# Kernel tuning notes

Measured on AMD Instinct MI355X. Metric: run time of the kernel, lower is better.

Reference implementation:

```python
import jax, jax.numpy as jnp
import numpy as np

H = 1024      # hidden_size
V = 50257     # output_size (vocab)
L = 512       # max_length


def setup_inputs() -> dict:
    key = jax.random.key(0)
    ks = jax.random.split(key, 12)
    s = 0.02
    return {
        "x": jax.random.randint(ks[0], (1,), 0, V),
        "encoder_outputs": jax.random.normal(ks[1], (L, H), jnp.float32),
        "hidden": jax.random.normal(ks[2], (1, 1, H), jnp.float32),
        # parameters
        "emb": jax.random.normal(ks[3], (V, H), jnp.float32) * s,
        "attn_W": jax.random.normal(ks[4], (L, 2 * H), jnp.float32) * s,
        "attn_b": jnp.zeros((L,), jnp.float32),
        "comb_W": jax.random.normal(ks[5], (H, 2 * H), jnp.float32) * s,
        "comb_b": jnp.zeros((H,), jnp.float32),
        "W_ih": jax.random.normal(ks[6], (3 * H, H), jnp.float32) * s,
        "W_hh": jax.random.normal(ks[7], (3 * H, H), jnp.float32) * s,
        "b_ih": jnp.zeros((3 * H,), jnp.float32),
        "b_hh": jnp.zeros((3 * H,), jnp.float32),
        "out_W": jax.random.normal(ks[8], (V, H), jnp.float32) * s,
        "out_b": jnp.zeros((V,), jnp.float32),
    }


def reference(x, encoder_outputs, hidden, emb, attn_W, attn_b, comb_W, comb_b,
              W_ih, W_hh, b_ih, b_hh, out_W, out_b):
    # embedded: [1, H]  (dropout_p=0 -> identity)
    embedded = emb[x]
    h0 = hidden[0]  # [1, H]
    # Bahdanau-style attention over encoder positions
    attn_weights = jax.nn.softmax(
        jnp.concatenate([embedded, h0], axis=1) @ attn_W.T + attn_b, axis=1)  # [1, L]
    attn_applied = attn_weights @ encoder_outputs  # [1, H]
    # combine + relu
    out = jnp.concatenate([embedded, attn_applied], axis=1) @ comb_W.T + comb_b
    out = jax.nn.relu(out)  # [1, H] -- GRU input
    # GRU cell (PyTorch gate ordering: r, z, n)
    gx = out @ W_ih.T + b_ih   # [1, 3H]
    gh = h0 @ W_hh.T + b_hh    # [1, 3H]
    gx_r, gx_z, gx_n = jnp.split(gx, 3, axis=1)
    gh_r, gh_z, gh_n = jnp.split(gh, 3, axis=1)
    r = jax.nn.sigmoid(gx_r + gh_r)
    z = jax.nn.sigmoid(gx_z + gh_z)
    n = jnp.tanh(gx_n + r * gh_n)
    h_new = (1.0 - z) * n + z * h0  # [1, H]
    # output projection + log_softmax
    logp = jax.nn.log_softmax(h_new @ out_W.T + out_b, axis=1)  # [1, V]
    return logp, attn_weights
```

## Files before the change

kernel.cpp:

```cpp
#include <hip/hip_runtime.h>
#include <math.h>

#define H 1024
#define V 50257
#define L 512

__device__ inline float wave_reduce_sum(float v) {
    #pragma unroll
    for (int off = 32; off > 0; off >>= 1)
        v += __shfl_down(v, off, 64);
    return v;
}

__device__ inline float wave_reduce_max(float v) {
    #pragma unroll
    for (int off = 32; off > 0; off >>= 1)
        v = fmaxf(v, __shfl_down(v, off, 64));
    return v;
}

__global__ void scores_kernel(const int* __restrict__ x,
                              const float* __restrict__ emb,
                              const float* __restrict__ hidden,
                              const float* __restrict__ attn_W,
                              const float* __restrict__ attn_b,
                              float* __restrict__ scores) {
    const int l = blockIdx.x;
    const int t = threadIdx.x;
    const int xi = x[0];
    const float* wrow = attn_W + (size_t)l * (2 * H);
    float acc = 0.f;
    #pragma unroll
    for (int k = 0; k < 8; ++k) {
        int j = t + k * 256;
        float a = (j < H) ? emb[(size_t)xi * H + j] : hidden[j - H];
        acc += a * wrow[j];
    }
    __shared__ float sm[4];
    acc = wave_reduce_sum(acc);
    if ((t & 63) == 0) sm[t >> 6] = acc;
    __syncthreads();
    if (t == 0)
        scores[l] = sm[0] + sm[1] + sm[2] + sm[3] + attn_b[l];
}

__global__ void softmax512(const float* __restrict__ scores,
                           float* __restrict__ attnw,
                           float* __restrict__ out_attn) {
    const int t = threadIdx.x;
    __shared__ float sm[8];
    float v = scores[t];
    float m = wave_reduce_max(v);
    if ((t & 63) == 0) sm[t >> 6] = m;
    __syncthreads();
    float M = sm[0];
    #pragma unroll
    for (int i = 1; i < 8; ++i) M = fmaxf(M, sm[i]);
    float e = expf(v - M);
    __syncthreads();
    float s = wave_reduce_sum(e);
    if ((t & 63) == 0) sm[t >> 6] = s;
    __syncthreads();
    float S = 0.f;
    #pragma unroll
    for (int i = 0; i < 8; ++i) S += sm[i];
    float w = e / S;
    attnw[t] = w;
    out_attn[t] = w;
}

__global__ void attn_apply(const float* __restrict__ attnw,
                           const float* __restrict__ enc,
                           float* __restrict__ attnap) {
    const int h = blockIdx.x * blockDim.x + threadIdx.x;
    float acc = 0.f;
    for (int l = 0; l < L; ++l)
        acc += attnw[l] * enc[(size_t)l * H + h];
    attnap[h] = acc;
}

__global__ void combine_relu(const int* __restrict__ x,
                             const float* __restrict__ emb,
                             const float* __restrict__ attnap,
                             const float* __restrict__ comb_W,
                             const float* __restrict__ comb_b,
                             float* __restrict__ gru_in) {
    const int r = blockIdx.x;
    const int t = threadIdx.x;
    const int xi = x[0];
    const float* wrow = comb_W + (size_t)r * (2 * H);
    float acc = 0.f;
    #pragma unroll
    for (int k = 0; k < 8; ++k) {
        int j = t + k * 256;
        float a = (j < H) ? emb[(size_t)xi * H + j] : attnap[j - H];
        acc += a * wrow[j];
    }
    __shared__ float sm[4];
    acc = wave_reduce_sum(acc);
    if ((t & 63) == 0) sm[t >> 6] = acc;
    __syncthreads();
    if (t == 0)
        gru_in[r] = fmaxf(sm[0] + sm[1] + sm[2] + sm[3] + comb_b[r], 0.f);
}

__global__ void gates_kernel(const float* __restrict__ W_ih,
                             const float* __restrict__ W_hh,
                             const float* __restrict__ b_ih,
                             const float* __restrict__ b_hh,
                             const float* __restrict__ gru_in,
                             const float* __restrict__ hidden,
                             float* __restrict__ gx,
                             float* __restrict__ gh) {
    const int b = blockIdx.x;
    const int t = threadIdx.x;
    const float* w;
    const float* vec;
    float bias;
    float* outp;
    int r;
    if (b < 3 * H) {
        r = b; w = W_ih + (size_t)r * H; vec = gru_in; bias = b_ih[r]; outp = gx;
    } else {
        r = b - 3 * H; w = W_hh + (size_t)r * H; vec = hidden; bias = b_hh[r]; outp = gh;
    }
    float acc = 0.f;
    #pragma unroll
    for (int k = 0; k < 4; ++k) {
        int j = t + k * 256;
        acc += vec[j] * w[j];
    }
    __shared__ float sm[4];
    acc = wave_reduce_sum(acc);
    if ((t & 63) == 0) sm[t >> 6] = acc;
    __syncthreads();
    if (t == 0)
        outp[r] = sm[0] + sm[1] + sm[2] + sm[3] + bias;
}

__global__ void gru_cell(const float* __restrict__ gx,
                         const float* __restrict__ gh,
                         const float* __restrict__ hidden,
                         float* __restrict__ h_new) {
    const int i = blockIdx.x * blockDim.x + threadIdx.x;
    float r = 1.f / (1.f + expf(-(gx[i] + gh[i])));
    float z = 1.f / (1.f + expf(-(gx[H + i] + gh[H + i])));
    float n = tanhf(gx[2 * H + i] + r * gh[2 * H + i]);
    h_new[i] = (1.f - z) * n + z * hidden[i];
}

__global__ void logits_kernel(const float* __restrict__ out_W,
                              const float* __restrict__ out_b,
                              const float* __restrict__ h_new,
                              float* __restrict__ logits) {
    const int lid = threadIdx.x & 63;
    const int wid = threadIdx.x >> 6;
    const int v = blockIdx.x * 4 + wid;
    if (v >= V) return;
    const float4* wrow = (const float4*)(out_W + (size_t)v * H);
    const float4* hv = (const float4*)h_new;
    float acc = 0.f;
    #pragma unroll
    for (int it = 0; it < 4; ++it) {
        int idx = it * 64 + lid;
        float4 w = wrow[idx];
        float4 h = hv[idx];
        acc += w.x * h.x + w.y * h.y + w.z * h.z + w.w * h.w;
    }
    acc = wave_reduce_sum(acc);
    if (lid == 0)
        logits[v] = acc + out_b[v];
}

__global__ void logsumexp_kernel(const float* __restrict__ logits,
                                 float* __restrict__ red) {
    const int t = threadIdx.x;
    __shared__ float sm[16];
    float m = -INFINITY;
    for (int v = t; v < V; v += 1024) m = fmaxf(m, logits[v]);
    m = wave_reduce_max(m);
    if ((t & 63) == 0) sm[t >> 6] = m;
    __syncthreads();
    float M = sm[0];
    #pragma unroll
    for (int i = 1; i < 16; ++i) M = fmaxf(M, sm[i]);
    __syncthreads();
    float s = 0.f;
    for (int v = t; v < V; v += 1024) s += expf(logits[v] - M);
    s = wave_reduce_sum(s);
    if ((t & 63) == 0) sm[t >> 6] = s;
    __syncthreads();
    if (t == 0) {
        float S = 0.f;
        #pragma unroll
        for (int i = 0; i < 16; ++i) S += sm[i];
        red[0] = M + logf(S);
    }
}

__global__ void finalize_kernel(float* __restrict__ logits,
                                const float* __restrict__ red) {
    const int v = blockIdx.x * blockDim.x + threadIdx.x;
    if (v < V) logits[v] -= red[0];
}

extern "C" void kernel_launch(void* const* d_in, const int* in_sizes, int n_in,
                              void* d_out, int out_size, void* d_ws, size_t ws_size,
                              hipStream_t stream) {
    const int*   x       = (const int*)d_in[0];
    const float* enc     = (const float*)d_in[1];
    const float* hidden  = (const float*)d_in[2];
    const float* emb     = (const float*)d_in[3];
    const float* attn_W  = (const float*)d_in[4];
    const float* attn_b  = (const float*)d_in[5];
    const float* comb_W  = (const float*)d_in[6];
    const float* comb_b  = (const float*)d_in[7];
    const float* W_ih    = (const float*)d_in[8];
    const float* W_hh    = (const float*)d_in[9];
    const float* b_ih    = (const float*)d_in[10];
    const float* b_hh    = (const float*)d_in[11];
    const float* out_W   = (const float*)d_in[12];
    const float* out_b   = (const float*)d_in[13];
    float* out = (float*)d_out;
    float* ws  = (float*)d_ws;

    float* scores = ws;
    float* attnw  = ws + 512;
    float* attnap = ws + 1024;
    float* gru_in = ws + 2048;
    float* gx     = ws + 3072;
    float* gh     = ws + 6144;
    float* h_new  = ws + 9216;
    float* red    = ws + 10240;

    scores_kernel<<<L, 256, 0, stream>>>(x, emb, hidden, attn_W, attn_b, scores);
    softmax512<<<1, L, 0, stream>>>(scores, attnw, out + V);
    attn_apply<<<H / 256, 256, 0, stream>>>(attnw, enc, attnap);
    combine_relu<<<H, 256, 0, stream>>>(x, emb, attnap, comb_W, comb_b, gru_in);
    gates_kernel<<<6 * H, 256, 0, stream>>>(W_ih, W_hh, b_ih, b_hh, gru_in, hidden, gx, gh);
    gru_cell<<<H / 256, 256, 0, stream>>>(gx, gh, hidden, h_new);
    logits_kernel<<<(V + 3) / 4, 256, 0, stream>>>(out_W, out_b, h_new, out);
    logsumexp_kernel<<<1, 1024, 0, stream>>>(out, red);
    finalize_kernel<<<(V + 255) / 256, 256, 0, stream>>>(out, red);
}
```

Measured before the change: 450.6 us.

## Fuse log-softmax partials into logits, split attention-apply over L, vectorize GEMVs

The logits kernel now computes 16 rows per block and writes a per-block (max, sum-exp) partial. This drops the single-block logsumexp pass over all 50K logits. Each finalize block reduces the ~3K partials redundantly and then subtracts the log-normalizer. attn_apply is split across 8 L-chunks with atomicAdd into a buffer that the softmax kernel zeroes, and the small GEMVs switch to float4 loads. The trade-offs are redundant partial reduction in every finalize block and nondeterministic float atomics.

```diff
diff --git a/kernel.cpp b/kernel.cpp
--- a/kernel.cpp
+++ b/kernel.cpp
@@ -4,6 +4,7 @@
 #define H 1024
 #define V 50257
 #define L 512
+#define NPART ((V + 15) / 16)
 
 __device__ inline float wave_reduce_sum(float v) {
     #pragma unroll
@@ -17,6 +18,10 @@
     for (int off = 32; off > 0; off >>= 1)
         v = fmaxf(v, __shfl_down(v, off, 64));
     return v;
+}
+
+__device__ inline float dot4(float4 a, float4 b) {
+    return a.x * b.x + a.y * b.y + a.z * b.z + a.w * b.w;
 }
 
 __global__ void scores_kernel(const int* __restrict__ x,
@@ -28,14 +33,10 @@
     const int l = blockIdx.x;
     const int t = threadIdx.x;
     const int xi = x[0];
-    const float* wrow = attn_W + (size_t)l * (2 * H);
-    float acc = 0.f;
-    #pragma unroll
-    for (int k = 0; k < 8; ++k) {
-        int j = t + k * 256;
-        float a = (j < H) ? emb[(size_t)xi * H + j] : hidden[j - H];
-        acc += a * wrow[j];
-    }
+    const float4* wrow = (const float4*)(attn_W + (size_t)l * (2 * H));
+    const float4* ev = (const float4*)(emb + (size_t)xi * H);
+    const float4* hv = (const float4*)hidden;
+    float acc = dot4(ev[t], wrow[t]) + dot4(hv[t], wrow[t + 256]);
     __shared__ float sm[4];
     acc = wave_reduce_sum(acc);
     if ((t & 63) == 0) sm[t >> 6] = acc;
@@ -46,8 +47,11 @@
 
 __global__ void softmax512(const float* __restrict__ scores,
                            float* __restrict__ attnw,
-                           float* __restrict__ out_attn) {
-    const int t = threadIdx.x;
+                           float* __restrict__ out_attn,
+                           float* __restrict__ attnap) {
+    const int t = threadIdx.x;
+    attnap[t] = 0.f;
+    attnap[t + 512] = 0.f;
     __shared__ float sm[8];
     float v = scores[t];
     float m = wave_reduce_max(v);
@@ -72,11 +76,13 @@
 __global__ void attn_apply(const float* __restrict__ attnw,
                            const float* __restrict__ enc,
                            float* __restrict__ attnap) {
-    const int h = blockIdx.x * blockDim.x + threadIdx.x;
+    const int h = blockIdx.x * 256 + threadIdx.x;
+    const int l0 = blockIdx.y * 64;
     float acc = 0.f;
-    for (int l = 0; l < L; ++l)
-        acc += attnw[l] * enc[(size_t)l * H + h];
-    attnap[h] = acc;
+    #pragma unroll 8
+    for (int i = 0; i < 64; ++i)
+        acc += attnw[l0 + i] * enc[(size_t)(l0 + i) * H + h];
+    atomicAdd(&attnap[h], acc);
 }
 
 __global__ void combine_relu(const int* __restrict__ x,
@@ -88,14 +94,10 @@
     const int r = blockIdx.x;
     const int t = threadIdx.x;
     const int xi = x[0];
-    const float* wrow = comb_W + (size_t)r * (2 * H);
-    float acc = 0.f;
-    #pragma unroll
-    for (int k = 0; k < 8; ++k) {
-        int j = t + k * 256;
-        float a = (j < H) ? emb[(size_t)xi * H + j] : attnap[j - H];
-        acc += a * wrow[j];
-    }
+    const float4* wrow = (const float4*)(comb_W + (size_t)r * (2 * H));
+    const float4* ev = (const float4*)(emb + (size_t)xi * H);
+    const float4* av = (const float4*)attnap;
+    float acc = dot4(ev[t], wrow[t]) + dot4(av[t], wrow[t + 256]);
     __shared__ float sm[4];
     acc = wave_reduce_sum(acc);
     if ((t & 63) == 0) sm[t >> 6] = acc;
@@ -124,12 +126,7 @@
     } else {
         r = b - 3 * H; w = W_hh + (size_t)r * H; vec = hidden; bias = b_hh[r]; outp = gh;
     }
-    float acc = 0.f;
-    #pragma unroll
-    for (int k = 0; k < 4; ++k) {
-        int j = t + k * 256;
-        acc += vec[j] * w[j];
-    }
+    float acc = dot4(((const float4*)vec)[t], ((const float4*)w)[t]);
     __shared__ float sm[4];
     acc = wave_reduce_sum(acc);
     if ((t & 63) == 0) sm[t >> 6] = acc;
@@ -152,56 +149,64 @@
 __global__ void logits_kernel(const float* __restrict__ out_W,
                               const float* __restrict__ out_b,
                               const float* __restrict__ h_new,
-                              float* __restrict__ logits) {
+                              float* __restrict__ logits,
+                              float* __restrict__ partials) {
     const int lid = threadIdx.x & 63;
     const int wid = threadIdx.x >> 6;
-    const int v = blockIdx.x * 4 + wid;
-    if (v >= V) return;
-    const float4* wrow = (const float4*)(out_W + (size_t)v * H);
+    __shared__ float sl[16];
     const float4* hv = (const float4*)h_new;
-    float acc = 0.f;
-    #pragma unroll
-    for (int it = 0; it < 4; ++it) {
-        int idx = it * 64 + lid;
-        float4 w = wrow[idx];
-        float4 h = hv[idx];
-        acc += w.x * h.x + w.y * h.y + w.z * h.z + w.w * h.w;
+    float4 h0 = hv[lid], h1 = hv[64 + lid], h2 = hv[128 + lid], h3 = hv[192 + lid];
+    const int vbase = blockIdx.x * 16 + wid * 4;
+    #pragma unroll
+    for (int rr = 0; rr < 4; ++rr) {
+        const int v = vbase + rr;
+        float val = -INFINITY;
+        if (v < V) {
+            const float4* wr = (const float4*)(out_W + (size_t)v * H);
+            float acc = dot4(wr[lid], h0) + dot4(wr[64 + lid], h1)
+                      + dot4(wr[128 + lid], h2) + dot4(wr[192 + lid], h3);
+            acc = wave_reduce_sum(acc);
+            if (lid == 0) { val = acc + out_b[v]; logits[v] = val; }
+        }
+        if (lid == 0) sl[wid * 4 + rr] = val;
     }
-    acc = wave_reduce_sum(acc);
-    if (lid == 0)
-        logits[v] = acc + out_b[v];
-}
-
-__global__ void logsumexp_kernel(const float* __restrict__ logits,
-                                 float* __restrict__ red) {
-    const int t = threadIdx.x;
-    __shared__ float sm[16];
+    __syncthreads();
+    if (threadIdx.x == 0) {
+        float M = -INFINITY;
+        #pragma unroll
+        for (int i = 0; i < 16; ++i) M = fmaxf(M, sl[i]);
+        float S = 0.f;
+        #pragma unroll
+        for (int i = 0; i < 16; ++i) S += expf(sl[i] - M);
+        partials[2 * blockIdx.x] = M;
+        partials[2 * blockIdx.x + 1] = S;
+    }
+}
+
+__global__ void finalize_kernel(float* __restrict__ logits,
+                                const float* __restrict__ partials) {
+    const int t = threadIdx.x;
+    __shared__ float sm[8];
     float m = -INFINITY;
-    for (int v = t; v < V; v += 1024) m = fmaxf(m, logits[v]);
+    for (int i = t; i < NPART; i += 512) m = fmaxf(m, partials[2 * i]);
     m = wave_reduce_max(m);
     if ((t & 63) == 0) sm[t >> 6] = m;
     __syncthreads();
     float M = sm[0];
     #pragma unroll
-    for (int i = 1; i < 16; ++i) M = fmaxf(M, sm[i]);
+    for (int i = 1; i < 8; ++i) M = fmaxf(M, sm[i]);
     __syncthreads();
     float s = 0.f;
-    for (int v = t; v < V; v += 1024) s += expf(logits[v] - M);
+    for (int i = t; i < NPART; i += 512) s += partials[2 * i + 1] * expf(partials[2 * i] - M);
     s = wave_reduce_sum(s);
     if ((t & 63) == 0) sm[t >> 6] = s;
     __syncthreads();
-    if (t == 0) {
-        float S = 0.f;
-        #pragma unroll
-        for (int i = 0; i < 16; ++i) S += sm[i];
-        red[0] = M + logf(S);
-    }
-}
-
-__global__ void finalize_kernel(float* __restrict__ logits,
-                                const float* __restrict__ red) {
-    const int v = blockIdx.x * blockDim.x + threadIdx.x;
-    if (v < V) logits[v] -= red[0];
+    float S = 0.f;
+    #pragma unroll
+    for (int i = 0; i < 8; ++i) S += sm[i];
+    const float red = M + logf(S);
+    const int v = blockIdx.x * 512 + t;
+    if (v < V) logits[v] -= red;
 }
 
 extern "C" void kernel_launch(void* const* d_in, const int* in_sizes, int n_in,
@@ -224,22 +229,21 @@
     float* out = (float*)d_out;
     float* ws  = (float*)d_ws;
 
-    float* scores = ws;
-    float* attnw  = ws + 512;
-    float* attnap = ws + 1024;
-    float* gru_in = ws + 2048;
-    float* gx     = ws + 3072;
-    float* gh     = ws + 6144;
-    float* h_new  = ws + 9216;
-    float* red    = ws + 10240;
+    float* scores   = ws;
+    float* attnw    = ws + 512;
+    float* attnap   = ws + 1024;
+    float* gru_in   = ws + 2048;
+    float* gx       = ws + 3072;
+    float* gh       = ws + 6144;
+    float* h_new    = ws + 9216;
+    float* partials = ws + 10240;
 
     scores_kernel<<<L, 256, 0, stream>>>(x, emb, hidden, attn_W, attn_b, scores);
-    softmax512<<<1, L, 0, stream>>>(scores, attnw, out + V);
-    attn_apply<<<H / 256, 256, 0, stream>>>(attnw, enc, attnap);
+    softmax512<<<1, L, 0, stream>>>(scores, attnw, out + V, attnap);
+    attn_apply<<<dim3(4, 8), 256, 0, stream>>>(attnw, enc, attnap);
     combine_relu<<<H, 256, 0, stream>>>(x, emb, attnap, comb_W, comb_b, gru_in);
     gates_kernel<<<6 * H, 256, 0, stream>>>(W_ih, W_hh, b_ih, b_hh, gru_in, hidden, gx, gh);
     gru_cell<<<H / 256, 256, 0, stream>>>(gx, gh, hidden, h_new);
-    logits_kernel<<<(V + 3) / 4, 256, 0, stream>>>(out_W, out_b, h_new, out);
-    logsumexp_kernel<<<1, 1024, 0, stream>>>(out, red);
-    finalize_kernel<<<(V + 255) / 256, 256, 0, stream>>>(out, red);
-}
+    logits_kernel<<<NPART, 256, 0, stream>>>(out_W, out_b, h_new, out, partials);
+    finalize_kernel<<<(V + 511) / 512, 512, 0, stream>>>(out, partials);
+}
```

Measured after the change: 425.3 us. 1.06x faster.
